# Optimization experiments

Measured on AMD Instinct MI355X. Metric: run time of the kernel, lower is better.

The kernel has to match this reference:

```python
import jax, jax.numpy as jnp
import numpy as np
from jax import lax

MAX_FEATURES = 50000
WIDTH = 256
EMBED = 2 * WIDTH
NUM_CLASS = 2
BATCH = 64
SEQ = 512


def setup_inputs() -> dict:
    key = jax.random.key(0)
    ks = jax.random.split(key, 10)
    s = lambda *shape: 1.0 / np.sqrt(shape[0])
    tokens = jax.random.randint(ks[0], (BATCH, SEQ), 0, MAX_FEATURES, dtype=jnp.int32)
    emb = jax.random.normal(ks[1], (MAX_FEATURES, EMBED), jnp.float32) * 0.05
    W1 = jax.random.normal(ks[2], (EMBED, WIDTH), jnp.float32) * s(EMBED)
    U1 = jax.random.normal(ks[3], (WIDTH, WIDTH), jnp.float32) * s(WIDTH)
    b1 = jnp.zeros((WIDTH,), jnp.float32)
    W2 = jax.random.normal(ks[4], (WIDTH, WIDTH), jnp.float32) * s(WIDTH)
    U2 = jax.random.normal(ks[5], (WIDTH, WIDTH), jnp.float32) * s(WIDTH)
    b2 = jnp.zeros((WIDTH,), jnp.float32)
    Wd = jax.random.normal(ks[6], (WIDTH, NUM_CLASS), jnp.float32) * s(WIDTH)
    bd = jnp.zeros((NUM_CLASS,), jnp.float32)
    return {"tokens": tokens, "emb": emb, "W1": W1, "U1": U1, "b1": b1,
            "W2": W2, "U2": U2, "b2": b2, "Wd": Wd, "bd": bd}


def _simple_rnn(x, W, U, b, return_sequences):
    # x: [B, S, D] -> precompute input projection once (big GEMM), then scan
    B = x.shape[0]
    H = U.shape[0]
    xw = jnp.einsum('bsd,dh->bsh', x, W) + b  # [B, S, H]
    def step(h, xt):
        h_new = jnp.tanh(xt + h @ U)
        return h_new, h_new
    h0 = jnp.zeros((B, H), x.dtype)
    h_last, hs = lax.scan(step, h0, jnp.swapaxes(xw, 0, 1))  # hs: [S, B, H]
    if return_sequences:
        return jnp.swapaxes(hs, 0, 1)  # [B, S, H]
    return h_last  # [B, H]


def reference(tokens, emb, W1, U1, b1, W2, U2, b2, Wd, bd):
    x = emb[tokens]                                  # [B, S, 2W] embedding lookup
    h1 = _simple_rnn(x, W1, U1, b1, return_sequences=True)   # [B, S, W]
    h2 = _simple_rnn(h1, W2, U2, b2, return_sequences=False)  # [B, W]
    logits = h2 @ Wd + bd                            # [B, num_class]
    return jax.nn.softmax(logits, axis=-1)
```

## Files before the change

### kernel.cpp

```cpp
#include <hip/hip_runtime.h>

typedef __attribute__((ext_vector_type(8))) short bf16x8;
typedef __attribute__((ext_vector_type(4))) float f32x4;

static __device__ __forceinline__ unsigned short f2bf(float x) {
    unsigned int u = __float_as_uint(x);
    u += 0x7fffu + ((u >> 16) & 1u);
    return (unsigned short)(u >> 16);
}

static __device__ __forceinline__ void barrier_lds_only() {
    __asm__ volatile("s_waitcnt lgkmcnt(0)\n\ts_barrier" ::: "memory");
}

__global__ void transpose4(const float* __restrict__ s0, const float* __restrict__ s1,
                           const float* __restrict__ s2, const float* __restrict__ s3,
                           unsigned short* __restrict__ d0, unsigned short* __restrict__ d1,
                           unsigned short* __restrict__ d2, unsigned short* __restrict__ d3) {
    int which = blockIdx.y;
    const float* src = which == 0 ? s0 : which == 1 ? s1 : which == 2 ? s2 : s3;
    unsigned short* dst = which == 0 ? d0 : which == 1 ? d1 : which == 2 ? d2 : d3;
    int K = (which == 0) ? 512 : 256;
    int idx = blockIdx.x * 256 + threadIdx.x;
    if (idx >= K * 256) return;
    int k = idx >> 8;
    int n = idx & 255;
    dst[n * K + k] = f2bf(src[idx]);
}

template<bool GATHER>
__global__ __launch_bounds__(256, 4) void gemm_mfma(
    const void* __restrict__ Aptr, const int* __restrict__ tokens,
    const unsigned short* __restrict__ Bt, const float* __restrict__ bias,
    float* __restrict__ C, int M, int N, int K)
{
    const int bn0 = blockIdx.x * 64;
    const int m0  = blockIdx.y * 64;
    const int tid = threadIdx.x;

    __shared__ unsigned short As[64 * 40];
    __shared__ unsigned short Bs[64 * 40];
    __shared__ int tok[64];

    if (GATHER) {
        if (tid < 64) tok[tid] = tokens[m0 + tid];
        __syncthreads();
    }

    const int r  = tid >> 2;
    const int c0 = (tid & 3) * 8;
    const int w  = tid >> 6;
    const int L  = tid & 63;
    const int ml = L & 15;
    const int q  = L >> 4;
    const int kq = q * 8;

    f32x4 acc[4] = {};

    for (int k0 = 0; k0 < K; k0 += 32) {
        unsigned short tmp[8];
        if (GATHER) {
            const float* src = (const float*)Aptr + (size_t)tok[r] * K + k0 + c0;
            float4 f0 = *(const float4*)(src);
            float4 f1 = *(const float4*)(src + 4);
            tmp[0]=f2bf(f0.x); tmp[1]=f2bf(f0.y); tmp[2]=f2bf(f0.z); tmp[3]=f2bf(f0.w);
            tmp[4]=f2bf(f1.x); tmp[5]=f2bf(f1.y); tmp[6]=f2bf(f1.z); tmp[7]=f2bf(f1.w);
        } else {
            const unsigned short* src = (const unsigned short*)Aptr + (size_t)(m0 + r) * K + k0 + c0;
            *(uint4*)tmp = *(const uint4*)src;
        }
        *(uint4*)&As[r * 40 + c0] = *(const uint4*)tmp;
        *(uint4*)&Bs[r * 40 + c0] = *(const uint4*)(Bt + (size_t)(bn0 + r) * K + k0 + c0);
        __syncthreads();

        bf16x8 av = *(const bf16x8*)&As[(16 * w + ml) * 40 + kq];
#pragma unroll
        for (int ns = 0; ns < 4; ++ns) {
            bf16x8 bv = *(const bf16x8*)&Bs[(ns * 16 + ml) * 40 + kq];
            acc[ns] = __builtin_amdgcn_mfma_f32_16x16x32_bf16(av, bv, acc[ns], 0, 0, 0);
        }
        __syncthreads();
    }

#pragma unroll
    for (int ns = 0; ns < 4; ++ns) {
        int gn = bn0 + ns * 16 + ml;
        float bv = bias[gn];
#pragma unroll
        for (int rr = 0; rr < 4; ++rr) {
            int gm = m0 + 16 * w + q * 4 + rr;
            C[(size_t)gm * N + gn] = acc[ns][rr] + bv;
        }
    }
}

template<bool SEQ>
__global__ __launch_bounds__(256, 1) void rnn_scan_mfma(
    const float* __restrict__ xw,
    const unsigned short* __restrict__ Ut,
    unsigned short* __restrict__ out_seq,
    float* __restrict__ out_last)
{
    const int b   = blockIdx.x;
    const int tid = threadIdx.x;
    const int w   = tid >> 6;
    const int L   = tid & 63;
    const int col = w * 64 + L;
    const int q   = L >> 4;
    const int ml  = L & 15;

    __shared__ unsigned short hsh[2][256];

    bf16x8 ufrag[4][8];
#pragma unroll
    for (int i = 0; i < 4; ++i) {
        const unsigned short* up = Ut + (size_t)((w * 4 + i) * 16 + ml) * 256 + q * 8;
#pragma unroll
        for (int kt = 0; kt < 8; ++kt)
            ufrag[i][kt] = *(const bf16x8*)(up + kt * 32);
    }

    hsh[0][tid] = 0;

    const float* xb = xw + (size_t)b * 512 * 256 + col;
    unsigned short* op = SEQ ? out_seq + (size_t)b * 512 * 256 + col : nullptr;

    float xq0 = xb[0 * 256];
    float xq1 = xb[1 * 256];
    float xq2 = xb[2 * 256];
    float xq3 = xb[3 * 256];
    const float* xpf = xb + 4 * 256;

    float lastv = 0.f;
    __syncthreads();

#define SCAN_STEP(CUR, XQ, PF)                                                       \
    {                                                                                \
        bf16x8 af[8];                                                                \
        _Pragma("unroll")                                                            \
        for (int kt = 0; kt < 8; ++kt)                                               \
            af[kt] = *(const bf16x8*)&hsh[CUR][kt * 32 + q * 8];                     \
        float xnew = 0.f;                                                            \
        if (PF) { xnew = *xpf; xpf += 256; }                                         \
        f32x4 accA[4] = {}, accB[4] = {};                                            \
        _Pragma("unroll")                                                            \
        for (int kt = 0; kt < 8; kt += 2) {                                          \
            _Pragma("unroll")                                                        \
            for (int i = 0; i < 4; ++i)                                              \
                accA[i] = __builtin_amdgcn_mfma_f32_16x16x32_bf16(af[kt], ufrag[i][kt], accA[i], 0, 0, 0);       \
            _Pragma("unroll")                                                        \
            for (int i = 0; i < 4; ++i)                                              \
                accB[i] = __builtin_amdgcn_mfma_f32_16x16x32_bf16(af[kt + 1], ufrag[i][kt + 1], accB[i], 0, 0, 0); \
        }                                                                            \
        float zA = (q == 0) ? accA[0][0] : (q == 1) ? accA[1][0] : (q == 2) ? accA[2][0] : accA[3][0]; \
        float zB = (q == 0) ? accB[0][0] : (q == 1) ? accB[1][0] : (q == 2) ? accB[2][0] : accB[3][0]; \
        float z  = zA + zB + XQ;                                                     \
        float e  = __expf(2.f * z);                  \
        float hn = 1.f - 2.f * __builtin_amdgcn_rcpf(e + 1.f);                       \
        lastv = hn;                                                                  \
        unsigned short hb = f2bf(hn);                                                \
        hsh[(CUR) ^ 1][col] = hb;                                                    \
        if (SEQ) { *op = hb; op += 256; }                                            \
        XQ = xnew;                                                                   \
        barrier_lds_only();                                                         \
    }

    for (int tt = 0; tt < 508; tt += 4) {
        SCAN_STEP(0, xq0, 1)
        SCAN_STEP(1, xq1, 1)
        SCAN_STEP(0, xq2, 1)
        SCAN_STEP(1, xq3, 1)
    }
    SCAN_STEP(0, xq0, 0)
    SCAN_STEP(1, xq1, 0)
    SCAN_STEP(0, xq2, 0)
    SCAN_STEP(1, xq3, 0)
#undef SCAN_STEP

    if (!SEQ) out_last[b * 256 + col] = lastv;
}

__global__ void head_kernel(const float* __restrict__ h2, const float* __restrict__ Wd,
                            const float* __restrict__ bd, float* __restrict__ out)
{
    int tid = threadIdx.x;
    int b = tid >> 1, c = tid & 1;
    float s = bd[c];
    for (int jj = 0; jj < 256; ++jj) s = fmaf(h2[b * 256 + jj], Wd[jj * 2 + c], s);
    __shared__ float lg[128];
    lg[tid] = s;
    __syncthreads();
    float o0 = lg[b * 2 + 0], o1 = lg[b * 2 + 1];
    float m = fmaxf(o0, o1);
    float z = __expf(o0 - m) + __expf(o1 - m);
    out[tid] = __expf(s - m) * __builtin_amdgcn_rcpf(z);
}

extern "C" void kernel_launch(void* const* d_in, const int* in_sizes, int n_in,
                              void* d_out, int out_size, void* d_ws, size_t ws_size,
                              hipStream_t stream) {
    const int*   tokens = (const int*)d_in[0];
    const float* emb    = (const float*)d_in[1];
    const float* W1     = (const float*)d_in[2];
    const float* U1     = (const float*)d_in[3];
    const float* b1     = (const float*)d_in[4];
    const float* W2     = (const float*)d_in[5];
    const float* U2     = (const float*)d_in[6];
    const float* b2     = (const float*)d_in[7];
    const float* Wd     = (const float*)d_in[8];
    const float* bd     = (const float*)d_in[9];
    float* out = (float*)d_out;

    char* ws = (char*)d_ws;
    float*          xw  = (float*)ws;
    unsigned short* h1  = (unsigned short*)(ws + (33554432));
    char*           p   = ws + 33554432 + 16777216;
    unsigned short* W1t = (unsigned short*)p;            p += 512 * 256 * 2;
    unsigned short* W2t = (unsigned short*)p;            p += 256 * 256 * 2;
    unsigned short* U1t = (unsigned short*)p;            p += 256 * 256 * 2;
    unsigned short* U2t = (unsigned short*)p;            p += 256 * 256 * 2;
    float*          h2  = (float*)p;

    const int M = 64 * 512;

    transpose4<<<dim3(512, 4), 256, 0, stream>>>(W1, W2, U1, U2, W1t, W2t, U1t, U2t);

    gemm_mfma<true><<<dim3(256 / 64, M / 64), 256, 0, stream>>>(
        emb, tokens, W1t, b1, xw, M, 256, 512);

    rnn_scan_mfma<true><<<64, 256, 0, stream>>>(xw, U1t, h1, nullptr);

    gemm_mfma<false><<<dim3(256 / 64, M / 64), 256, 0, stream>>>(
        h1, nullptr, W2t, b2, xw, M, 256, 256);

    rnn_scan_mfma<false><<<64, 256, 0, stream>>>(xw, U2t, nullptr, h2);

    head_kernel<<<1, 128, 0, stream>>>(h2, Wd, bd, out);
}
```

Measured before the change: 660.1 us.

## Split recurrent matvec over K across waves with LDS partial-sum reduction

Result: slower. 924.8 us (+40.1%).

```diff
diff --git a/kernel.cpp b/kernel.cpp
--- a/kernel.cpp
+++ b/kernel.cpp
@@ -105,25 +105,32 @@
     const int tid = threadIdx.x;
     const int w   = tid >> 6;
     const int L   = tid & 63;
-    const int col = w * 64 + L;
     const int q   = L >> 4;
     const int ml  = L & 15;
 
-    __shared__ unsigned short hsh[2][256];
-
-    bf16x8 ufrag[4][8];
-#pragma unroll
-    for (int i = 0; i < 4; ++i) {
-        const unsigned short* up = Ut + (size_t)((w * 4 + i) * 16 + ml) * 256 + q * 8;
-#pragma unroll
-        for (int kt = 0; kt < 8; ++kt)
-            ufrag[i][kt] = *(const bf16x8*)(up + kt * 32);
-    }
-
-    hsh[0][tid] = 0;
-
-    const float* xb = xw + (size_t)b * 512 * 256 + col;
-    unsigned short* op = SEQ ? out_seq + (size_t)b * 512 * 256 + col : nullptr;
+    __shared__ unsigned short hsh[256];
+    __shared__ float part[4][256];
+
+    bf16x8 ufrag[16][2];
+#pragma unroll
+    for (int i = 0; i < 16; ++i) {
+        const unsigned short* up = Ut + (size_t)(i * 16 + ml) * 256 + w * 64 + q * 8;
+        ufrag[i][0] = *(const bf16x8*)(up);
+        ufrag[i][1] = *(const bf16x8*)(up + 32);
+    }
+
+    hsh[tid] = 0;
+
+    const unsigned short* ha0 = &hsh[w * 64 + q * 8];
+    const unsigned short* ha1 = &hsh[w * 64 + 32 + q * 8];
+
+    float* pw0 = &part[w][(4 * 0 + q) * 16 + ml];
+    float* pw1 = &part[w][(4 * 1 + q) * 16 + ml];
+    float* pw2 = &part[w][(4 * 2 + q) * 16 + ml];
+    float* pw3 = &part[w][(4 * 3 + q) * 16 + ml];
+
+    const float* xb = xw + (size_t)b * 512 * 256 + tid;
+    unsigned short* op = SEQ ? out_seq + (size_t)b * 512 * 256 + tid : nullptr;
 
     float xq0 = xb[0 * 256];
     float xq1 = xb[1 * 256];
@@ -131,53 +138,54 @@
     float xq3 = xb[3 * 256];
     const float* xpf = xb + 4 * 256;
 
+    const f32x4 zf = {0.f, 0.f, 0.f, 0.f};
     float lastv = 0.f;
     __syncthreads();
 
-#define SCAN_STEP(CUR, XQ, PF)                                                       \
+#define SCAN_STEP(XQ, PF)                                                            \
     {                                                                                \
-        bf16x8 af[8];                                                                \
-        _Pragma("unroll")                                                            \
-        for (int kt = 0; kt < 8; ++kt)                                               \
-            af[kt] = *(const bf16x8*)&hsh[CUR][kt * 32 + q * 8];                     \
+        bf16x8 af0 = *(const bf16x8*)ha0;                                            \
+        bf16x8 af1 = *(const bf16x8*)ha1;                                            \
         float xnew = 0.f;                                                            \
         if (PF) { xnew = *xpf; xpf += 256; }                                         \
-        f32x4 accA[4] = {}, accB[4] = {};                                            \
+        f32x4 acc[16];                                                               \
         _Pragma("unroll")                                                            \
-        for (int kt = 0; kt < 8; kt += 2) {                                          \
-            _Pragma("unroll")                                                        \
-            for (int i = 0; i < 4; ++i)                                              \
-                accA[i] = __builtin_amdgcn_mfma_f32_16x16x32_bf16(af[kt], ufrag[i][kt], accA[i], 0, 0, 0);       \
-            _Pragma("unroll")                                                        \
-            for (int i = 0; i < 4; ++i)                                              \
-                accB[i] = __builtin_amdgcn_mfma_f32_16x16x32_bf16(af[kt + 1], ufrag[i][kt + 1], accB[i], 0, 0, 0); \
-        }                                                                            \
-        float zA = (q == 0) ? accA[0][0] : (q == 1) ? accA[1][0] : (q == 2) ? accA[2][0] : accA[3][0]; \
-        float zB = (q == 0) ? accB[0][0] : (q == 1) ? accB[1][0] : (q == 2) ? accB[2][0] : accB[3][0]; \
-        float z  = zA + zB + XQ;                                                     \
+        for (int i = 0; i < 16; ++i)                                                 \
+            acc[i] = __builtin_amdgcn_mfma_f32_16x16x32_bf16(af0, ufrag[i][0], zf, 0, 0, 0); \
+        _Pragma("unroll")                                                            \
+        for (int i = 0; i < 16; ++i)                                                 \
+            acc[i] = __builtin_amdgcn_mfma_f32_16x16x32_bf16(af1, ufrag[i][1], acc[i], 0, 0, 0); \
+        float v0 = (q == 0) ? acc[0][0]  : (q == 1) ? acc[1][0]  : (q == 2) ? acc[2][0]  : acc[3][0];  \
+        float v1 = (q == 0) ? acc[4][0]  : (q == 1) ? acc[5][0]  : (q == 2) ? acc[6][0]  : acc[7][0];  \
+        float v2 = (q == 0) ? acc[8][0]  : (q == 1) ? acc[9][0]  : (q == 2) ? acc[10][0] : acc[11][0]; \
+        float v3 = (q == 0) ? acc[12][0] : (q == 1) ? acc[13][0] : (q == 2) ? acc[14][0] : acc[15][0]; \
+        *pw0 = v0; *pw1 = v1; *pw2 = v2; *pw3 = v3;                                  \
+        barrier_lds_only();                                    \
+        float p0 = part[0][tid], p1 = part[1][tid], p2 = part[2][tid], p3 = part[3][tid]; \
+        float z = ((p0 + p1) + (p2 + p3)) + XQ;                                      \
         float e  = __expf(2.f * z);                  \
         float hn = 1.f - 2.f * __builtin_amdgcn_rcpf(e + 1.f);                       \
         lastv = hn;                                                                  \
         unsigned short hb = f2bf(hn);                                                \
-        hsh[(CUR) ^ 1][col] = hb;                                                    \
+        hsh[tid] = hb;                                                               \
         if (SEQ) { *op = hb; op += 256; }                                            \
         XQ = xnew;                                                                   \
-        barrier_lds_only();                                                         \
+        barrier_lds_only();                          \
     }
 
     for (int tt = 0; tt < 508; tt += 4) {
-        SCAN_STEP(0, xq0, 1)
-        SCAN_STEP(1, xq1, 1)
-        SCAN_STEP(0, xq2, 1)
-        SCAN_STEP(1, xq3, 1)
-    }
-    SCAN_STEP(0, xq0, 0)
-    SCAN_STEP(1, xq1, 0)
-    SCAN_STEP(0, xq2, 0)
-    SCAN_STEP(1, xq3, 0)
+        SCAN_STEP(xq0, 1)
+        SCAN_STEP(xq1, 1)
+        SCAN_STEP(xq2, 1)
+        SCAN_STEP(xq3, 1)
+    }
+    SCAN_STEP(xq0, 0)
+    SCAN_STEP(xq1, 0)
+    SCAN_STEP(xq2, 0)
+    SCAN_STEP(xq3, 0)
 #undef SCAN_STEP
 
-    if (!SEQ) out_last[b * 256 + col] = lastv;
+    if (!SEQ) out_last[b * 256 + tid] = lastv;
 }
 
 __global__ void head_kernel(const float* __restrict__ h2, const float* __restrict__ Wd,
```

## Batch four sequences per RNN scan block to fill MFMA rows

Applied to the files above, without the earlier changes.

Result: slower. 738.4 us (+11.9%).

```diff
diff --git a/kernel.cpp b/kernel.cpp
--- a/kernel.cpp
+++ b/kernel.cpp
@@ -101,37 +101,44 @@
     unsigned short* __restrict__ out_seq,
     float* __restrict__ out_last)
 {
-    const int b   = blockIdx.x;
+    const int b0  = blockIdx.x * 4;
     const int tid = threadIdx.x;
-    const int w   = tid >> 6;
+    const int wl  = tid >> 6;
     const int L   = tid & 63;
-    const int col = w * 64 + L;
     const int q   = L >> 4;
     const int ml  = L & 15;
 
-    __shared__ unsigned short hsh[2][256];
+    __shared__ unsigned short hsh[2][4][272];
 
     bf16x8 ufrag[4][8];
 #pragma unroll
     for (int i = 0; i < 4; ++i) {
-        const unsigned short* up = Ut + (size_t)((w * 4 + i) * 16 + ml) * 256 + q * 8;
+        const unsigned short* up = Ut + (size_t)((wl * 4 + i) * 16 + ml) * 256 + q * 8;
 #pragma unroll
         for (int kt = 0; kt < 8; ++kt)
             ufrag[i][kt] = *(const bf16x8*)(up + kt * 32);
     }
 
-    hsh[0][tid] = 0;
-
-    const float* xb = xw + (size_t)b * 512 * 256 + col;
-    unsigned short* op = SEQ ? out_seq + (size_t)b * 512 * 256 + col : nullptr;
-
-    float xq0 = xb[0 * 256];
-    float xq1 = xb[1 * 256];
-    float xq2 = xb[2 * 256];
-    float xq3 = xb[3 * 256];
-    const float* xpf = xb + 4 * 256;
-
-    float lastv = 0.f;
+    for (int i = tid; i < 4 * 272; i += 256) ((unsigned short*)hsh[0])[i] = 0;
+
+    const unsigned short* ha[2] = { &hsh[0][ml >> 2][q * 8], &hsh[1][ml >> 2][q * 8] };
+    unsigned short* hw[2] = { &hsh[0][q][wl * 64 + ml], &hsh[1][q][wl * 64 + ml] };
+
+    const float* xp = xw + (size_t)(b0 + q) * 512 * 256 + wl * 64 + ml;
+    unsigned short* op = SEQ ? out_seq + (size_t)(b0 + q) * 512 * 256 + wl * 64 + ml : nullptr;
+
+    float xq0[4], xq1[4], xq2[4], xq3[4];
+#pragma unroll
+    for (int nt = 0; nt < 4; ++nt) {
+        xq0[nt] = xp[0 * 256 + nt * 16];
+        xq1[nt] = xp[1 * 256 + nt * 16];
+        xq2[nt] = xp[2 * 256 + nt * 16];
+        xq3[nt] = xp[3 * 256 + nt * 16];
+    }
+    const float* xpf = xp + 4 * 256;
+
+    const f32x4 zf = {0.f, 0.f, 0.f, 0.f};
+    float lastv[4] = {0.f, 0.f, 0.f, 0.f};
     __syncthreads();
 
 #define SCAN_STEP(CUR, XQ, PF)                                                       \
@@ -139,12 +146,22 @@
         bf16x8 af[8];                                                                \
         _Pragma("unroll")                                                            \
         for (int kt = 0; kt < 8; ++kt)                                               \
-            af[kt] = *(const bf16x8*)&hsh[CUR][kt * 32 + q * 8];                     \
-        float xnew = 0.f;                                                            \
-        if (PF) { xnew = *xpf; xpf += 256; }                                         \
-        f32x4 accA[4] = {}, accB[4] = {};                                            \
-        _Pragma("unroll")                                                            \
-        for (int kt = 0; kt < 8; kt += 2) {                                          \
+            af[kt] = *(const bf16x8*)(ha[CUR] + kt * 32);                            \
+        float xn[4] = {0.f, 0.f, 0.f, 0.f};                                          \
+        if (PF) {                                                                    \
+            _Pragma("unroll")                                                        \
+            for (int nt = 0; nt < 4; ++nt) xn[nt] = xpf[nt * 16];                    \
+            xpf += 256;                                                              \
+        }                                                                            \
+        f32x4 accA[4], accB[4];                                                      \
+        _Pragma("unroll")                                                            \
+        for (int i = 0; i < 4; ++i)                                                  \
+            accA[i] = __builtin_amdgcn_mfma_f32_16x16x32_bf16(af[0], ufrag[i][0], zf, 0, 0, 0); \
+        _Pragma("unroll")                                                            \
+        for (int i = 0; i < 4; ++i)                                                  \
+            accB[i] = __builtin_amdgcn_mfma_f32_16x16x32_bf16(af[1], ufrag[i][1], zf, 0, 0, 0); \
+        _Pragma("unroll")                                                            \
+        for (int kt = 2; kt < 8; kt += 2) {                                          \
             _Pragma("unroll")                                                        \
             for (int i = 0; i < 4; ++i)                                              \
                 accA[i] = __builtin_amdgcn_mfma_f32_16x16x32_bf16(af[kt], ufrag[i][kt], accA[i], 0, 0, 0);       \
@@ -152,17 +169,27 @@
             for (int i = 0; i < 4; ++i)                                              \
                 accB[i] = __builtin_amdgcn_mfma_f32_16x16x32_bf16(af[kt + 1], ufrag[i][kt + 1], accB[i], 0, 0, 0); \
         }                                                                            \
-        float zA = (q == 0) ? accA[0][0] : (q == 1) ? accA[1][0] : (q == 2) ? accA[2][0] : accA[3][0]; \
-        float zB = (q == 0) ? accB[0][0] : (q == 1) ? accB[1][0] : (q == 2) ? accB[2][0] : accB[3][0]; \
-        float z  = zA + zB + XQ;                                                     \
-        float e  = __expf(2.f * z);                  \
-        float hn = 1.f - 2.f * __builtin_amdgcn_rcpf(e + 1.f);                       \
-        lastv = hn;                                                                  \
-        unsigned short hb = f2bf(hn);                                                \
-        hsh[(CUR) ^ 1][col] = hb;                                                    \
-        if (SEQ) { *op = hb; op += 256; }                                            \
-        XQ = xnew;                                                                   \
-        barrier_lds_only();                                                         \
+        unsigned short hb[4];                                                        \
+        _Pragma("unroll")                                                            \
+        for (int nt = 0; nt < 4; ++nt) {                                             \
+            float z = accA[nt][0] + accB[nt][0] + XQ[nt];                            \
+            float e = __expf(2.f * z);               \
+            float hn = 1.f - 2.f * __builtin_amdgcn_rcpf(e + 1.f);                   \
+            lastv[nt] = hn;                                                          \
+            hb[nt] = f2bf(hn);                                                       \
+        }                                                                            \
+        _Pragma("unroll")                                                            \
+        for (int nt = 0; nt < 4; ++nt) hw[(CUR) ^ 1][nt * 16] = hb[nt];              \
+        if (SEQ) {                                                                   \
+            _Pragma("unroll")                                                        \
+            for (int nt = 0; nt < 4; ++nt) op[nt * 16] = hb[nt];                     \
+            op += 256;                                                               \
+        }                                                                            \
+        if (PF) {                                                                    \
+            _Pragma("unroll")                                                        \
+            for (int nt = 0; nt < 4; ++nt) XQ[nt] = xn[nt];                          \
+        }                                                                            \
+        barrier_lds_only();                       \
     }
 
     for (int tt = 0; tt < 508; tt += 4) {
@@ -177,7 +204,11 @@
     SCAN_STEP(1, xq3, 0)
 #undef SCAN_STEP
 
-    if (!SEQ) out_last[b * 256 + col] = lastv;
+    if (!SEQ) {
+#pragma unroll
+        for (int nt = 0; nt < 4; ++nt)
+            out_last[(b0 + q) * 256 + wl * 64 + nt * 16 + ml] = lastv[nt];
+    }
 }
 
 __global__ void head_kernel(const float* __restrict__ h2, const float* __restrict__ Wd,
@@ -228,12 +259,12 @@
     gemm_mfma<true><<<dim3(256 / 64, M / 64), 256, 0, stream>>>(
         emb, tokens, W1t, b1, xw, M, 256, 512);
 
-    rnn_scan_mfma<true><<<64, 256, 0, stream>>>(xw, U1t, h1, nullptr);
+    rnn_scan_mfma<true><<<16, 256, 0, stream>>>(xw, U1t, h1, nullptr);
 
     gemm_mfma<false><<<dim3(256 / 64, M / 64), 256, 0, stream>>>(
         h1, nullptr, W2t, b2, xw, M, 256, 256);
 
-    rnn_scan_mfma<false><<<64, 256, 0, stream>>>(xw, U2t, nullptr, h2);
+    rnn_scan_mfma<false><<<16, 256, 0, stream>>>(xw, U2t, nullptr, h2);
 
     head_kernel<<<1, 128, 0, stream>>>(h2, Wd, bd, out);
 }
```

## Store GEMM output time-major per column and vector-prefetch inputs in RNN scan

Applied to the files above, without the earlier changes.

Result: slower. 684.6 us (+3.7%).

```diff
diff --git a/kernel.cpp b/kernel.cpp
--- a/kernel.cpp
+++ b/kernel.cpp
@@ -82,21 +82,20 @@
         __syncthreads();
     }
 
+    const int bb    = m0 >> 9;
+    const int tbase = (m0 & 511) + 16 * w + q * 4;
 #pragma unroll
     for (int ns = 0; ns < 4; ++ns) {
         int gn = bn0 + ns * 16 + ml;
         float bv = bias[gn];
-#pragma unroll
-        for (int rr = 0; rr < 4; ++rr) {
-            int gm = m0 + 16 * w + q * 4 + rr;
-            C[(size_t)gm * N + gn] = acc[ns][rr] + bv;
-        }
+        float4 v = { acc[ns][0] + bv, acc[ns][1] + bv, acc[ns][2] + bv, acc[ns][3] + bv };
+        *(float4*)&C[(size_t)bb * 131072 + (size_t)gn * 512 + tbase] = v;
     }
 }
 
 template<bool SEQ>
 __global__ __launch_bounds__(256, 1) void rnn_scan_mfma(
-    const float* __restrict__ xw,
+    const float* __restrict__ xwT,
     const unsigned short* __restrict__ Ut,
     unsigned short* __restrict__ out_seq,
     float* __restrict__ out_last)
@@ -122,29 +121,31 @@
 
     hsh[0][tid] = 0;
 
-    const float* xb = xw + (size_t)b * 512 * 256 + col;
+    const float* xb = xwT + (size_t)b * 131072 + (size_t)col * 512;
     unsigned short* op = SEQ ? out_seq + (size_t)b * 512 * 256 + col : nullptr;
 
-    float xq0 = xb[0 * 256];
-    float xq1 = xb[1 * 256];
-    float xq2 = xb[2 * 256];
-    float xq3 = xb[3 * 256];
-    const float* xpf = xb + 4 * 256;
-
+    float4 cch0 = *(const float4*)(xb);
+    float4 cch1 = *(const float4*)(xb + 4);
+
+    const f32x4 zf = {0.f, 0.f, 0.f, 0.f};
     float lastv = 0.f;
     __syncthreads();
 
-#define SCAN_STEP(CUR, XQ, PF)                                                       \
+#define SCAN_STEP(CUR, XV)                                                           \
     {                                                                                \
         bf16x8 af[8];                                                                \
         _Pragma("unroll")                                                            \
         for (int kt = 0; kt < 8; ++kt)                                               \
             af[kt] = *(const bf16x8*)&hsh[CUR][kt * 32 + q * 8];                     \
-        float xnew = 0.f;                                                            \
-        if (PF) { xnew = *xpf; xpf += 256; }                                         \
-        f32x4 accA[4] = {}, accB[4] = {};                                            \
-        _Pragma("unroll")                                                            \
-        for (int kt = 0; kt < 8; kt += 2) {                                          \
+        f32x4 accA[4], accB[4];                                                      \
+        _Pragma("unroll")                                                            \
+        for (int i = 0; i < 4; ++i)                                                  \
+            accA[i] = __builtin_amdgcn_mfma_f32_16x16x32_bf16(af[0], ufrag[i][0], zf, 0, 0, 0); \
+        _Pragma("unroll")                                                            \
+        for (int i = 0; i < 4; ++i)                                                  \
+            accB[i] = __builtin_amdgcn_mfma_f32_16x16x32_bf16(af[1], ufrag[i][1], zf, 0, 0, 0); \
+        _Pragma("unroll")                                                            \
+        for (int kt = 2; kt < 8; kt += 2) {                                          \
             _Pragma("unroll")                                                        \
             for (int i = 0; i < 4; ++i)                                              \
                 accA[i] = __builtin_amdgcn_mfma_f32_16x16x32_bf16(af[kt], ufrag[i][kt], accA[i], 0, 0, 0);       \
@@ -154,27 +155,42 @@
         }                                                                            \
         float zA = (q == 0) ? accA[0][0] : (q == 1) ? accA[1][0] : (q == 2) ? accA[2][0] : accA[3][0]; \
         float zB = (q == 0) ? accB[0][0] : (q == 1) ? accB[1][0] : (q == 2) ? accB[2][0] : accB[3][0]; \
-        float z  = zA + zB + XQ;                                                     \
+        float z  = zA + zB + (XV);                                                   \
         float e  = __expf(2.f * z);                  \
         float hn = 1.f - 2.f * __builtin_amdgcn_rcpf(e + 1.f);                       \
         lastv = hn;                                                                  \
         unsigned short hb = f2bf(hn);                                                \
         hsh[(CUR) ^ 1][col] = hb;                                                    \
         if (SEQ) { *op = hb; op += 256; }                                            \
-        XQ = xnew;                                                                   \
-        barrier_lds_only();                                                         \
-    }
-
-    for (int tt = 0; tt < 508; tt += 4) {
-        SCAN_STEP(0, xq0, 1)
-        SCAN_STEP(1, xq1, 1)
-        SCAN_STEP(0, xq2, 1)
-        SCAN_STEP(1, xq3, 1)
-    }
-    SCAN_STEP(0, xq0, 0)
-    SCAN_STEP(1, xq1, 0)
-    SCAN_STEP(0, xq2, 0)
-    SCAN_STEP(1, xq3, 0)
+        barrier_lds_only();                       \
+    }
+
+    for (int g = 0; g < 126; g += 2) {
+        {
+            float4 nx = *(const float4*)(xb + 4 * g + 8);
+            SCAN_STEP(0, cch0.x)
+            SCAN_STEP(1, cch0.y)
+            SCAN_STEP(0, cch0.z)
+            SCAN_STEP(1, cch0.w)
+            cch0 = nx;
+        }
+        {
+            float4 nx = *(const float4*)(xb + 4 * g + 12);
+            SCAN_STEP(0, cch1.x)
+            SCAN_STEP(1, cch1.y)
+            SCAN_STEP(0, cch1.z)
+            SCAN_STEP(1, cch1.w)
+            cch1 = nx;
+        }
+    }
+    SCAN_STEP(0, cch0.x)
+    SCAN_STEP(1, cch0.y)
+    SCAN_STEP(0, cch0.z)
+    SCAN_STEP(1, cch0.w)
+    SCAN_STEP(0, cch1.x)
+    SCAN_STEP(1, cch1.y)
+    SCAN_STEP(0, cch1.z)
+    SCAN_STEP(1, cch1.w)
 #undef SCAN_STEP
 
     if (!SEQ) out_last[b * 256 + col] = lastv;
@@ -212,7 +228,7 @@
     float* out = (float*)d_out;
 
     char* ws = (char*)d_ws;
-    float*          xw  = (float*)ws;
+    float*          xwT = (float*)ws;
     unsigned short* h1  = (unsigned short*)(ws + (33554432));
     char*           p   = ws + 33554432 + 16777216;
     unsigned short* W1t = (unsigned short*)p;            p += 512 * 256 * 2;
@@ -226,14 +242,14 @@
     transpose4<<<dim3(512, 4), 256, 0, stream>>>(W1, W2, U1, U2, W1t, W2t, U1t, U2t);
 
     gemm_mfma<true><<<dim3(256 / 64, M / 64), 256, 0, stream>>>(
-        emb, tokens, W1t, b1, xw, M, 256, 512);
-
-    rnn_scan_mfma<true><<<64, 256, 0, stream>>>(xw, U1t, h1, nullptr);
+        emb, tokens, W1t, b1, xwT, M, 256, 512);
+
+    rnn_scan_mfma<true><<<64, 256, 0, stream>>>(xwT, U1t, h1, nullptr);
 
     gemm_mfma<false><<<dim3(256 / 64, M / 64), 256, 0, stream>>>(
-        h1, nullptr, W2t, b2, xw, M, 256, 256);
-
-    rnn_scan_mfma<false><<<64, 256, 0, stream>>>(xw, U2t, nullptr, h2);
+        h1, nullptr, W2t, b2, xwT, M, 256, 256);
+
+    rnn_scan_mfma<false><<<64, 256, 0, stream>>>(xwT, U2t, nullptr, h2);
 
     head_kernel<<<1, 128, 0, stream>>>(h2, Wd, bd, out);
 }
```
